# Kernel tuning notes

Measured on AMD Instinct MI355X. Metric: run time of the kernel, lower is better.

Reference implementation:

```python
import jax, jax.numpy as jnp
import numpy as np

B, N, M = 64, 4096, 128
TOTAL_LABELS = 21
TOTAL_POS = 128
TOTAL_NEG = 128
VARIANCES = jnp.array([0.1, 0.1, 0.2, 0.2], dtype=jnp.float32)


def _make_boxes(key, b, n):
    # valid [y1, x1, y2, x2] boxes in [0, 1]
    k1, k2 = jax.random.split(key)
    c1 = jax.random.uniform(k1, (b, n, 2), dtype=jnp.float32)
    c2 = jax.random.uniform(k2, (b, n, 2), dtype=jnp.float32)
    lo = jnp.minimum(c1, c2)
    hi = jnp.maximum(c1, c2)
    return jnp.concatenate([lo, hi], axis=-1)


def setup_inputs() -> dict:
    key = jax.random.key(0)
    k1, k2, k3 = jax.random.split(key, 3)
    roi_bboxes = _make_boxes(k1, B, N)
    gt_boxes = _make_boxes(k2, B, M)
    gt_labels = jax.random.randint(k3, (B, M), 0, TOTAL_LABELS, dtype=jnp.int32)
    return {"roi_bboxes": roi_bboxes, "gt_boxes": gt_boxes, "gt_labels": gt_labels}


def generate_iou(bboxes, gt_boxes):
    # bboxes: [B,N,4], gt_boxes: [B,M,4]; format [y1,x1,y2,x2] -> iou [B,N,M]
    by1, bx1, by2, bx2 = jnp.split(bboxes, 4, axis=-1)      # each [B,N,1]
    gy1, gx1, gy2, gx2 = jnp.split(gt_boxes, 4, axis=-1)    # each [B,M,1]
    gt_area = ((gy2 - gy1) * (gx2 - gx1))[..., 0]           # [B,M]
    bbox_area = ((by2 - by1) * (bx2 - bx1))[..., 0]         # [B,N]
    x_top = jnp.maximum(bx1, jnp.swapaxes(gx1, 1, 2))       # [B,N,M]
    y_top = jnp.maximum(by1, jnp.swapaxes(gy1, 1, 2))
    x_bot = jnp.minimum(bx2, jnp.swapaxes(gx2, 1, 2))
    y_bot = jnp.minimum(by2, jnp.swapaxes(gy2, 1, 2))
    inter = jnp.maximum(x_bot - x_top, 0.0) * jnp.maximum(y_bot - y_top, 0.0)
    union = bbox_area[:, :, None] + gt_area[:, None, :] - inter
    return inter / union


def randomly_select_mask(key, mask, count):
    # keep at most `count` True entries per row, chosen at random (rpn_utils.randomly_select_xyz_mask)
    rand = jax.random.randint(key, mask.shape, 1, count * 10, dtype=jnp.int32)
    mult = mask.astype(jnp.int32) * rand
    order = jnp.argsort(-mult, axis=1)       # descending sort of masked random scores
    rank = jnp.argsort(order, axis=1)        # rank of each element in that order
    return mask & (rank < count)


def bbox_to_delta(bboxes, gt_boxes):
    bw = bboxes[..., 3] - bboxes[..., 1]
    bh = bboxes[..., 2] - bboxes[..., 0]
    bcx = bboxes[..., 1] + 0.5 * bw
    bcy = bboxes[..., 0] + 0.5 * bh
    gw = gt_boxes[..., 3] - gt_boxes[..., 1]
    gh = gt_boxes[..., 2] - gt_boxes[..., 0]
    gcx = gt_boxes[..., 1] + 0.5 * gw
    gcy = gt_boxes[..., 0] + 0.5 * gh
    bw = jnp.where(bw == 0.0, 1e-3, bw)
    bh = jnp.where(bh == 0.0, 1e-3, bh)
    dx = (gcx - bcx) / bw
    dy = (gcy - bcy) / bh
    gw_safe = jnp.where(gw == 0.0, 1.0, gw)  # avoid nan grads through masked log
    gh_safe = jnp.where(gh == 0.0, 1.0, gh)
    dw = jnp.where(gw == 0.0, 0.0, jnp.log(gw_safe / bw))
    dh = jnp.where(gh == 0.0, 0.0, jnp.log(gh_safe / bh))
    return jnp.stack([dy, dx, dh, dw], axis=-1)


def _forward(roi_bboxes, gt_boxes, gt_labels):
    kp, kn = jax.random.split(jax.random.key(42))
    iou_map = generate_iou(roi_bboxes, gt_boxes)             # [B,N,M]
    max_idx = jnp.argmax(iou_map, axis=2)                    # [B,N]
    merged = jnp.max(iou_map, axis=2)                        # [B,N]
    pos_mask = randomly_select_mask(kp, merged > 0.5, TOTAL_POS)
    neg_mask = randomly_select_mask(kn, (merged < 0.5) & (merged > 0.1), TOTAL_NEG)
    # batched gather of best-matching gt box / label per roi
    gt_boxes_map = jnp.take_along_axis(gt_boxes, max_idx[..., None], axis=1)   # [B,N,4]
    gt_labels_map = jnp.take_along_axis(gt_labels, max_idx, axis=1)            # [B,N]
    expanded_gt_boxes = jnp.where(pos_mask[..., None], gt_boxes_map, 0.0)
    pos_gt_labels = jnp.where(pos_mask, gt_labels_map, -1)
    expanded_gt_labels = pos_gt_labels  # hyper_params['background'] == False
    deltas = bbox_to_delta(roi_bboxes, expanded_gt_boxes) / VARIANCES           # [B,N,4]
    labels_oh = jax.nn.one_hot(expanded_gt_labels, TOTAL_LABELS, dtype=deltas.dtype)  # [B,N,L]; -1 -> all zeros
    roi_bbox_deltas = labels_oh[..., None] * deltas[..., None, :]               # [B,N,L,4]
    return roi_bbox_deltas, labels_oh


def reference(roi_bboxes, gt_boxes, gt_labels):
    return _forward(roi_bboxes, gt_boxes, gt_labels)
```

## Files before the change

### kernel.cpp

```cpp
#include <hip/hip_runtime.h>
#include <stdint.h>

#pragma clang fp contract(off)


#define BB 64
#define NN 4096
#define MM 128
#define LL 21
#define NTOT (BB * NN)
#define DELTA_ELEMS ((size_t)BB * NN * LL * 4)

__host__ __device__ __forceinline__ uint32_t rotl32(uint32_t v, int s) {
  return (v << s) | (v >> (32 - s));
}

__host__ __device__ inline void threefry2x32(uint32_t k0, uint32_t k1,
                                             uint32_t x0, uint32_t x1,
                                             uint32_t* o0, uint32_t* o1) {
  const uint32_t ks2 = k0 ^ k1 ^ 0x1BD11BDAu;
  x0 += k0; x1 += k1;
#define TF_R(r) do { x0 += x1; x1 = rotl32(x1, (r)); x1 ^= x0; } while (0)
  TF_R(13); TF_R(15); TF_R(26); TF_R(6);
  x0 += k1;  x1 += ks2 + 1u;
  TF_R(17); TF_R(29); TF_R(16); TF_R(24);
  x0 += ks2; x1 += k0 + 2u;
  TF_R(13); TF_R(15); TF_R(26); TF_R(6);
  x0 += k0;  x1 += k1 + 3u;
  TF_R(17); TF_R(29); TF_R(16); TF_R(24);
  x0 += k1;  x1 += ks2 + 4u;
  TF_R(13); TF_R(15); TF_R(26); TF_R(6);
  x0 += ks2; x1 += k0 + 5u;
#undef TF_R
  *o0 = x0; *o1 = x1;
}

__device__ __forceinline__ uint32_t jax_bits32(uint32_t ka, uint32_t kb, uint32_t idx) {
  uint32_t o0, o1;
  threefry2x32(ka, kb, 0u, idx, &o0, &o1);
  return o0 ^ o1;
}

__device__ __forceinline__ uint32_t jax_randint_1_1280(uint32_t k1a, uint32_t k1b,
                                                       uint32_t k2a, uint32_t k2b,
                                                       uint32_t idx) {
  const uint32_t hi = jax_bits32(k1a, k1b, idx);
  const uint32_t lo = jax_bits32(k2a, k2b, idx);
  const uint32_t off = ((hi % 1279u) * 882u + (lo % 1279u)) % 1279u;
  return 1u + off;
}

__global__ __launch_bounds__(256) void iou_kernel(const float* __restrict__ roi,
                                                  const float* __restrict__ gt,
                                                  int* __restrict__ midx,
                                                  float* __restrict__ merged,
                                                  int stride) {
  __shared__ float4 gtb[MM];
  __shared__ float gar[MM];
  const int b = blockIdx.y;
  const int t = threadIdx.x;
  if (t < MM) {
    const float4 g = ((const float4*)gt)[b * MM + t];
    gtb[t] = g;
    gar[t] = (g.z - g.x) * (g.w - g.y);
  }
  __syncthreads();
  const int i = b * NN + blockIdx.x * 256 + t;
  const float4 r = ((const float4*)roi)[i];
  const float barea = (r.z - r.x) * (r.w - r.y);
  float best = -1.0f;
  int bm = 0;
  for (int m = 0; m < MM; ++m) {
    const float4 g = gtb[m];
    const float xt = fmaxf(r.y, g.y);
    const float yt = fmaxf(r.x, g.x);
    const float xb = fminf(r.w, g.w);
    const float yb = fminf(r.z, g.z);
    const float iw = fmaxf(xb - xt, 0.0f);
    const float ih = fmaxf(yb - yt, 0.0f);
    const float inter = iw * ih;
    const float uni = (barea + gar[m]) - inter;
    const float iou = inter / uni;
    if (iou > best) { best = iou; bm = m; }
  }
  midx[(size_t)i * stride] = bm;
  merged[(size_t)i * stride] = best;
}

__global__ __launch_bounds__(256) void select_kernel(const float* __restrict__ merged,
                                                     int* __restrict__ sel,
                                                     int stride,
                                                     uint32_t k1a, uint32_t k1b,
                                                     uint32_t k2a, uint32_t k2b) {
  __shared__ uint32_t buf[NN];
  __shared__ uint32_t hist[1280];
  __shared__ uint32_t scan[256];
  __shared__ int s_thr;
  __shared__ int s_take;
  const int b = blockIdx.x;
  const int t = threadIdx.x;
  for (int j = t; j < 1280; j += 256) hist[j] = 0u;
  if (t == 0) { s_thr = 0; s_take = 0; }
  #pragma unroll
  for (int k = 0; k < 16; ++k) {
    const int li = t + k * 256;
    buf[li] = __float_as_uint(merged[(size_t)(b * NN + li) * stride]);
  }
  __syncthreads();

  uint32_t rv[16];
  const int lbase = t * 16;
  #pragma unroll
  for (int k = 0; k < 16; ++k) {
    const int li = lbase + k;
    uint32_t r = 0u;
    if (__uint_as_float(buf[li]) > 0.5f) {
      r = jax_randint_1_1280(k1a, k1b, k2a, k2b, (uint32_t)(b * NN + li));
      atomicAdd(&hist[r], 1u);
    }
    rv[k] = r;
  }
  __syncthreads();

  uint32_t chunk = 0;
  #pragma unroll
  for (int j = 0; j < 5; ++j) chunk += hist[t * 5 + j];
  scan[t] = chunk;
  __syncthreads();
  for (int off = 1; off < 256; off <<= 1) {
    const uint32_t v = (t + off < 256) ? scan[t + off] : 0u;
    __syncthreads();
    scan[t] += v;
    __syncthreads();
  }
  const uint32_t total = scan[0];
  if (total > 128u) {
    const uint32_t Sc = scan[t];
    const uint32_t Sn = (t < 255) ? scan[t + 1] : 0u;
    if (Sc >= 128u && Sn < 128u) {
      uint32_t s = Sn;
      #pragma unroll
      for (int j = 4; j >= 0; --j) {
        const uint32_t h = hist[t * 5 + j];
        if (s + h >= 128u) { s_thr = t * 5 + j; s_take = 128 - (int)s; break; }
        s += h;
      }
    }
  }
  __syncthreads();
  const int thr = s_thr;
  const uint32_t take = (uint32_t)s_take;

  uint32_t lt = 0;
  if (thr > 0) {
    #pragma unroll
    for (int k = 0; k < 16; ++k) lt += (rv[k] == (uint32_t)thr) ? 1u : 0u;
  }
  scan[t] = lt;
  __syncthreads();
  for (int off = 1; off < 256; off <<= 1) {
    const uint32_t v = (t >= off) ? scan[t - off] : 0u;
    __syncthreads();
    scan[t] += v;
    __syncthreads();
  }
  uint32_t run = scan[t] - lt;

  #pragma unroll
  for (int k = 0; k < 16; ++k) {
    bool s;
    if (thr == 0) {
      s = rv[k] > 0u;
    } else {
      s = (rv[k] > (uint32_t)thr);
      if (rv[k] == (uint32_t)thr) { s = (run < take); ++run; }
    }
    buf[lbase + k] = s ? 1u : 0u;
  }
  __syncthreads();
  #pragma unroll
  for (int k = 0; k < 16; ++k) {
    const int li = t + k * 256;
    sel[(size_t)(b * NN + li) * stride] = (int)buf[li];
  }
}

__global__ __launch_bounds__(256) void out_kernel(const float* __restrict__ roi,
                                                  const float* __restrict__ gt,
                                                  const int* __restrict__ glab,
                                                  const int* __restrict__ midx,
                                                  const int* __restrict__ sel,
                                                  int stride,
                                                  float* __restrict__ out) {
  __shared__ float4 sdv[256];
  __shared__ int slbl[256];
  const int t = threadIdx.x;
  const int ri0 = blockIdx.x * 256;
  const int i = ri0 + t;
  const int b = i >> 12;
  const int mi = midx[(size_t)i * stride];
  const int sv = sel[(size_t)i * stride];
  float4 dv = {0.f, 0.f, 0.f, 0.f};
  int lbl = -1;
  if (sv) {
    const float4 r = ((const float4*)roi)[i];
    const float4 g = ((const float4*)gt)[b * MM + mi];
    lbl = glab[b * MM + mi];
    float bh = r.z - r.x, bw = r.w - r.y;
    const float bcy = r.x + 0.5f * bh, bcx = r.y + 0.5f * bw;
    const float gh = g.z - g.x, gw = g.w - g.y;
    const float gcy = g.x + 0.5f * gh, gcx = g.y + 0.5f * gw;
    if (bw == 0.0f) bw = 1e-3f;
    if (bh == 0.0f) bh = 1e-3f;
    const float dx = (gcx - bcx) / bw;
    const float dy = (gcy - bcy) / bh;
    const float dw = (gw == 0.0f) ? 0.0f : logf(gw / bw);
    const float dh = (gh == 0.0f) ? 0.0f : logf(gh / bh);
    dv.x = dy / 0.1f; dv.y = dx / 0.1f; dv.z = dh / 0.2f; dv.w = dw / 0.2f;
  }
  sdv[t] = dv;
  slbl[t] = lbl;
  __syncthreads();

  const float4 z = {0.f, 0.f, 0.f, 0.f};
  float4* dbase = (float4*)out + (size_t)ri0 * LL;
  #pragma unroll
  for (int k = 0; k < LL; ++k) {
    const int q = t + k * 256;
    const int r = q / 21;
    const int f = q - r * 21;
    dbase[q] = (f == slbl[r]) ? sdv[r] : z;
  }
  float4* lbase = (float4*)(out + DELTA_ELEMS) + (size_t)ri0 * LL / 4;
  for (int q = t; q < 1344; q += 256) {
    const int e0 = q * 4;
    float4 v;
    {
      const int r0 = e0 / 21;       v.x = ((e0 - r0 * 21) == slbl[r0]) ? 1.f : 0.f;
      const int r1 = (e0 + 1) / 21; v.y = ((e0 + 1 - r1 * 21) == slbl[r1]) ? 1.f : 0.f;
      const int r2 = (e0 + 2) / 21; v.z = ((e0 + 2 - r2 * 21) == slbl[r2]) ? 1.f : 0.f;
      const int r3 = (e0 + 3) / 21; v.w = ((e0 + 3 - r3 * 21) == slbl[r3]) ? 1.f : 0.f;
    }
    lbase[q] = v;
  }
}

extern "C" void kernel_launch(void* const* d_in, const int* in_sizes, int n_in,
                              void* d_out, int out_size, void* d_ws, size_t ws_size,
                              hipStream_t stream) {
  const float* roi = (const float*)d_in[0];
  const float* gt  = (const float*)d_in[1];
  const int* glab  = (const int*)d_in[2];
  float* out = (float*)d_out;

  uint32_t kp0, kp1, k1a, k1b, k2a, k2b;
  threefry2x32(0u, 42u, 0u, 0u, &kp0, &kp1);
  threefry2x32(kp0, kp1, 0u, 0u, &k1a, &k1b);
  threefry2x32(kp0, kp1, 0u, 1u, &k2a, &k2b);

  int* midx;
  float* merged;
  int* sel;
  int stride;
  if (d_ws != nullptr && ws_size >= (size_t)3 * NTOT * 4) {
    char* ws = (char*)d_ws;
    midx   = (int*)ws;
    merged = (float*)(ws + (size_t)NTOT * 4);
    sel    = (int*)(ws + (size_t)2 * NTOT * 4);
    stride = 1;
  } else {
    midx   = (int*)out;
    merged = out + 1;
    sel    = (int*)out + 2;
    stride = LL * 4;
  }

  hipLaunchKernelGGL(iou_kernel, dim3(NN / 256, BB), dim3(256), 0, stream,
                     roi, gt, midx, merged, stride);
  hipLaunchKernelGGL(select_kernel, dim3(BB), dim3(256), 0, stream,
                     merged, sel, stride, k1a, k1b, k2a, k2b);
  hipLaunchKernelGGL(out_kernel, dim3(NTOT / 256), dim3(256), 0, stream,
                     roi, gt, glab, midx, sel, stride, out);
}
```

Baseline: 64.45 us.

## Replace dense output kernel with zero-fill plus sparse scatter from selection

When a workspace is available, the selection and output stages are merged. A grid-stride zero-fill kernel clears the whole output buffer, and the selection kernel then scatters only the deltas and one-hot labels for the selected ROIs. This drops the intermediate selection-mask buffer and the per-element compare logic of the dense output kernel, leaving a simple streaming store of zeros. The scatter writes are uncoalesced, and the fill now runs as a separate launch before the 64-block selection kernel.

Result: slower. 79.27 us (+23.0%).

```diff
diff --git a/kernel.cpp b/kernel.cpp
--- a/kernel.cpp
+++ b/kernel.cpp
@@ -10,6 +10,8 @@
 #define LL 21
 #define NTOT (BB * NN)
 #define DELTA_ELEMS ((size_t)BB * NN * LL * 4)
+#define OUT_FLOATS (DELTA_ELEMS + (size_t)NTOT * LL)
+#define OUT_F4 (OUT_FLOATS / 4)
 
 __host__ __device__ __forceinline__ uint32_t rotl32(uint32_t v, int s) {
   return (v << s) | (v >> (32 - s));
@@ -50,6 +52,22 @@
   return 1u + off;
 }
 
+__device__ __forceinline__ float4 compute_delta(const float4 r, const float4 g) {
+  float bh = r.z - r.x, bw = r.w - r.y;
+  const float bcy = r.x + 0.5f * bh, bcx = r.y + 0.5f * bw;
+  const float gh = g.z - g.x, gw = g.w - g.y;
+  const float gcy = g.x + 0.5f * gh, gcx = g.y + 0.5f * gw;
+  if (bw == 0.0f) bw = 1e-3f;
+  if (bh == 0.0f) bh = 1e-3f;
+  const float dx = (gcx - bcx) / bw;
+  const float dy = (gcy - bcy) / bh;
+  const float dw = (gw == 0.0f) ? 0.0f : logf(gw / bw);
+  const float dh = (gh == 0.0f) ? 0.0f : logf(gh / bh);
+  float4 dv;
+  dv.x = dy / 0.1f; dv.y = dx / 0.1f; dv.z = dh / 0.2f; dv.w = dw / 0.2f;
+  return dv;
+}
+
 __global__ __launch_bounds__(256) void iou_kernel(const float* __restrict__ roi,
                                                   const float* __restrict__ gt,
                                                   int* __restrict__ midx,
@@ -87,6 +105,114 @@
   merged[(size_t)i * stride] = best;
 }
 
+__global__ __launch_bounds__(256) void zerofill_kernel(float4* __restrict__ out) {
+  const float4 z = {0.f, 0.f, 0.f, 0.f};
+  const size_t step = (size_t)gridDim.x * 256;
+  for (size_t q = (size_t)blockIdx.x * 256 + threadIdx.x; q < OUT_F4; q += step)
+    out[q] = z;
+}
+
+__global__ __launch_bounds__(256) void select_scatter_kernel(
+    const float* __restrict__ roi, const float* __restrict__ gt,
+    const int* __restrict__ glab, const int* __restrict__ midx,
+    const float* __restrict__ merged, float* __restrict__ out,
+    uint32_t k1a, uint32_t k1b, uint32_t k2a, uint32_t k2b) {
+  __shared__ uint32_t buf[NN];
+  __shared__ uint32_t hist[1280];
+  __shared__ uint32_t scan[256];
+  __shared__ int s_thr;
+  __shared__ int s_take;
+  const int b = blockIdx.x;
+  const int t = threadIdx.x;
+  for (int j = t; j < 1280; j += 256) hist[j] = 0u;
+  if (t == 0) { s_thr = 0; s_take = 0; }
+  #pragma unroll
+  for (int k = 0; k < 16; ++k) {
+    const int li = t + k * 256;
+    buf[li] = __float_as_uint(merged[b * NN + li]);
+  }
+  __syncthreads();
+
+  uint32_t rv[16];
+  const int lbase = t * 16;
+  #pragma unroll
+  for (int k = 0; k < 16; ++k) {
+    const int li = lbase + k;
+    uint32_t r = 0u;
+    if (__uint_as_float(buf[li]) > 0.5f) {
+      r = jax_randint_1_1280(k1a, k1b, k2a, k2b, (uint32_t)(b * NN + li));
+      atomicAdd(&hist[r], 1u);
+    }
+    rv[k] = r;
+  }
+  __syncthreads();
+
+  uint32_t chunk = 0;
+  #pragma unroll
+  for (int j = 0; j < 5; ++j) chunk += hist[t * 5 + j];
+  scan[t] = chunk;
+  __syncthreads();
+  for (int off = 1; off < 256; off <<= 1) {
+    const uint32_t v = (t + off < 256) ? scan[t + off] : 0u;
+    __syncthreads();
+    scan[t] += v;
+    __syncthreads();
+  }
+  const uint32_t total = scan[0];
+  if (total > 128u) {
+    const uint32_t Sc = scan[t];
+    const uint32_t Sn = (t < 255) ? scan[t + 1] : 0u;
+    if (Sc >= 128u && Sn < 128u) {
+      uint32_t s = Sn;
+      #pragma unroll
+      for (int j = 4; j >= 0; --j) {
+        const uint32_t h = hist[t * 5 + j];
+        if (s + h >= 128u) { s_thr = t * 5 + j; s_take = 128 - (int)s; break; }
+        s += h;
+      }
+    }
+  }
+  __syncthreads();
+  const int thr = s_thr;
+  const uint32_t take = (uint32_t)s_take;
+
+  uint32_t lt = 0;
+  if (thr > 0) {
+    #pragma unroll
+    for (int k = 0; k < 16; ++k) lt += (rv[k] == (uint32_t)thr) ? 1u : 0u;
+  }
+  scan[t] = lt;
+  __syncthreads();
+  for (int off = 1; off < 256; off <<= 1) {
+    const uint32_t v = (t >= off) ? scan[t - off] : 0u;
+    __syncthreads();
+    scan[t] += v;
+    __syncthreads();
+  }
+  uint32_t run = scan[t] - lt;
+
+  #pragma unroll
+  for (int k = 0; k < 16; ++k) {
+    bool s;
+    if (thr == 0) {
+      s = rv[k] > 0u;
+    } else {
+      s = (rv[k] > (uint32_t)thr);
+      if (rv[k] == (uint32_t)thr) { s = (run < take); ++run; }
+    }
+    if (s) {
+      const int i = b * NN + lbase + k;
+      const int mi = midx[i];
+      const float4 r = ((const float4*)roi)[i];
+      const float4 g = ((const float4*)gt)[b * MM + mi];
+      const int lbl = glab[b * MM + mi];
+      const float4 dv = compute_delta(r, g);
+      ((float4*)out)[(size_t)i * LL + lbl] = dv;
+      out[DELTA_ELEMS + (size_t)i * LL + lbl] = 1.0f;
+    }
+  }
+}
+
 __global__ __launch_bounds__(256) void select_kernel(const float* __restrict__ merged,
                                                      int* __restrict__ sel,
                                                      int stride,
@@ -107,7 +233,6 @@
     buf[li] = __float_as_uint(merged[(size_t)(b * NN + li) * stride]);
   }
   __syncthreads();
-
   uint32_t rv[16];
   const int lbase = t * 16;
   #pragma unroll
@@ -121,7 +246,6 @@
     rv[k] = r;
   }
   __syncthreads();
-
   uint32_t chunk = 0;
   #pragma unroll
   for (int j = 0; j < 5; ++j) chunk += hist[t * 5 + j];
@@ -150,7 +274,6 @@
   __syncthreads();
   const int thr = s_thr;
   const uint32_t take = (uint32_t)s_take;
-
   uint32_t lt = 0;
   if (thr > 0) {
     #pragma unroll
@@ -165,7 +288,6 @@
     __syncthreads();
   }
   uint32_t run = scan[t] - lt;
-
   #pragma unroll
   for (int k = 0; k < 16; ++k) {
     bool s;
@@ -206,22 +328,11 @@
     const float4 r = ((const float4*)roi)[i];
     const float4 g = ((const float4*)gt)[b * MM + mi];
     lbl = glab[b * MM + mi];
-    float bh = r.z - r.x, bw = r.w - r.y;
-    const float bcy = r.x + 0.5f * bh, bcx = r.y + 0.5f * bw;
-    const float gh = g.z - g.x, gw = g.w - g.y;
-    const float gcy = g.x + 0.5f * gh, gcx = g.y + 0.5f * gw;
-    if (bw == 0.0f) bw = 1e-3f;
-    if (bh == 0.0f) bh = 1e-3f;
-    const float dx = (gcx - bcx) / bw;
-    const float dy = (gcy - bcy) / bh;
-    const float dw = (gw == 0.0f) ? 0.0f : logf(gw / bw);
-    const float dh = (gh == 0.0f) ? 0.0f : logf(gh / bh);
-    dv.x = dy / 0.1f; dv.y = dx / 0.1f; dv.z = dh / 0.2f; dv.w = dw / 0.2f;
+    dv = compute_delta(r, g);
   }
   sdv[t] = dv;
   slbl[t] = lbl;
   __syncthreads();
-
   const float4 z = {0.f, 0.f, 0.f, 0.f};
   float4* dbase = (float4*)out + (size_t)ri0 * LL;
   #pragma unroll
@@ -235,12 +346,10 @@
   for (int q = t; q < 1344; q += 256) {
     const int e0 = q * 4;
     float4 v;
-    {
-      const int r0 = e0 / 21;       v.x = ((e0 - r0 * 21) == slbl[r0]) ? 1.f : 0.f;
-      const int r1 = (e0 + 1) / 21; v.y = ((e0 + 1 - r1 * 21) == slbl[r1]) ? 1.f : 0.f;
-      const int r2 = (e0 + 2) / 21; v.z = ((e0 + 2 - r2 * 21) == slbl[r2]) ? 1.f : 0.f;
-      const int r3 = (e0 + 3) / 21; v.w = ((e0 + 3 - r3 * 21) == slbl[r3]) ? 1.f : 0.f;
-    }
+    const int r0 = e0 / 21;       v.x = ((e0 - r0 * 21) == slbl[r0]) ? 1.f : 0.f;
+    const int r1 = (e0 + 1) / 21; v.y = ((e0 + 1 - r1 * 21) == slbl[r1]) ? 1.f : 0.f;
+    const int r2 = (e0 + 2) / 21; v.z = ((e0 + 2 - r2 * 21) == slbl[r2]) ? 1.f : 0.f;
+    const int r3 = (e0 + 3) / 21; v.w = ((e0 + 3 - r3 * 21) == slbl[r3]) ? 1.f : 0.f;
     lbase[q] = v;
   }
 }
@@ -258,27 +367,25 @@
   threefry2x32(kp0, kp1, 0u, 0u, &k1a, &k1b);
   threefry2x32(kp0, kp1, 0u, 1u, &k2a, &k2b);
 
-  int* midx;
-  float* merged;
-  int* sel;
-  int stride;
-  if (d_ws != nullptr && ws_size >= (size_t)3 * NTOT * 4) {
-    char* ws = (char*)d_ws;
-    midx   = (int*)ws;
-    merged = (float*)(ws + (size_t)NTOT * 4);
-    sel    = (int*)(ws + (size_t)2 * NTOT * 4);
-    stride = 1;
+  if (d_ws != nullptr && ws_size >= (size_t)2 * NTOT * 4) {
+    int* midx     = (int*)d_ws;
+    float* merged = (float*)((char*)d_ws + (size_t)NTOT * 4);
+    hipLaunchKernelGGL(iou_kernel, dim3(NN / 256, BB), dim3(256), 0, stream,
+                       roi, gt, midx, merged, 1);
+    hipLaunchKernelGGL(zerofill_kernel, dim3(2048), dim3(256), 0, stream,
+                       (float4*)out);
+    hipLaunchKernelGGL(select_scatter_kernel, dim3(BB), dim3(256), 0, stream,
+                       roi, gt, glab, midx, merged, out, k1a, k1b, k2a, k2b);
   } else {
-    midx   = (int*)out;
-    merged = out + 1;
-    sel    = (int*)out + 2;
-    stride = LL * 4;
-  }
-
-  hipLaunchKernelGGL(iou_kernel, dim3(NN / 256, BB), dim3(256), 0, stream,
-                     roi, gt, midx, merged, stride);
-  hipLaunchKernelGGL(select_kernel, dim3(BB), dim3(256), 0, stream,
-                     merged, sel, stride, k1a, k1b, k2a, k2b);
-  hipLaunchKernelGGL(out_kernel, dim3(NTOT / 256), dim3(256), 0, stream,
-                     roi, gt, glab, midx, sel, stride, out);
-}
+    int* midx     = (int*)out;
+    float* merged = out + 1;
+    int* sel      = (int*)out + 2;
+    const int stride = LL * 4;
+    hipLaunchKernelGGL(iou_kernel, dim3(NN / 256, BB), dim3(256), 0, stream,
+                       roi, gt, midx, merged, stride);
+    hipLaunchKernelGGL(select_kernel, dim3(BB), dim3(256), 0, stream,
+                       merged, sel, stride, k1a, k1b, k2a, k2b);
+    hipLaunchKernelGGL(out_kernel, dim3(NTOT / 256), dim3(256), 0, stream,
+                       roi, gt, glab, midx, sel, stride, out);
+  }
+}
```
